# Kernel optimization log

Hardware: AMD Instinct MI355X
Metric: run time of the kernel (lower is better)

The kernel has to match this reference:

```python
import jax, jax.numpy as jnp
import numpy as np

EPS = 1e-12  # torch spectral_norm default eps


def _l2norm(v):
    return v / (jnp.linalg.norm(v) + EPS)


def _spectral_norm_2d(w, u):
    # one power iteration (torch default n_power_iterations=1), u/v detached
    v = _l2norm(w.T @ u)
    u_new = _l2norm(w @ v)
    u_new = jax.lax.stop_gradient(u_new)
    v = jax.lax.stop_gradient(v)
    sigma = u_new @ (w @ v)
    return w / sigma


def _spectral_norm_1d(b):
    # torch._SpectralNorm for ndim==1: F.normalize(weight, dim=0)
    return b / (jnp.linalg.norm(b) + EPS)


def setup_inputs() -> dict:
    key = jax.random.key(0)
    ks = jax.random.split(key, 8)
    T, B, I, H = 4096, 32, 256, 256
    s_i = 1.0 / np.sqrt(H)  # nn.RNN init: U(-1/sqrt(H), 1/sqrt(H))
    return {
        "x": jax.random.normal(ks[0], (T, B, I), jnp.float32),
        "state": jax.random.normal(ks[1], (1, B, H), jnp.float32),
        "w_ih": jax.random.uniform(ks[2], (H, I), jnp.float32, -s_i, s_i),
        "w_hh": jax.random.uniform(ks[3], (H, H), jnp.float32, -s_i, s_i),
        "b_ih": jax.random.uniform(ks[4], (H,), jnp.float32, -s_i, s_i),
        "b_hh": jax.random.uniform(ks[5], (H,), jnp.float32, -s_i, s_i),
        "u_ih": jax.random.normal(ks[6], (H,), jnp.float32),  # power-iteration buffer
        "u_hh": jax.random.normal(ks[7], (H,), jnp.float32),
    }


def reference(x, state, w_ih, w_hh, b_ih, b_hh, u_ih, u_hh):
    # spectral-norm parametrization of all RNN weights
    w_ih_sn = _spectral_norm_2d(w_ih, _l2norm(u_ih))
    w_hh_sn = _spectral_norm_2d(w_hh, _l2norm(u_hh))
    b_sn = _spectral_norm_1d(b_ih) + _spectral_norm_1d(b_hh)

    # input projection batched over all timesteps: [T,B,H]
    pre = jnp.einsum("tbi,hi->tbh", x, w_ih_sn) + b_sn

    def step(h, p):
        h_new = jnp.tanh(p + h @ w_hh_sn.T)
        return h_new, h_new

    h_last, out = jax.lax.scan(step, state[0], pre)
    return out, h_last[None]
```

## Files before the change

kernel.cpp:

```cpp
#include <hip/hip_runtime.h>
#include <hip/hip_bf16.h>
#include <math.h>

#define EPSF 1e-12f
#define H 256
#define TSTEPS 4096
#define BATCH 32
#define TB (TSTEPS*BATCH)
#define BH (BATCH*H)

typedef _Float16 h2 __attribute__((ext_vector_type(2)));

#if defined(__has_builtin)
#if __has_builtin(__builtin_amdgcn_fdot2)
#define FDOT2(a, b, c) __builtin_amdgcn_fdot2((a), (b), (c), false)
#endif
#endif
#ifndef FDOT2
#define FDOT2(a, b, c) fmaf((float)(a).y, (float)(b).y, fmaf((float)(a).x, (float)(b).x, (c)))
#endif

#define BC(u) __builtin_bit_cast(h2, (u))

#define DPPF(x, ctrl) __builtin_bit_cast(float, __builtin_amdgcn_update_dpp( \
    0, __builtin_bit_cast(int, (x)), (ctrl), 0xf, 0xf, true))
#define DPP_QUAD_XOR1 0xB1
#define DPP_QUAD_XOR2 0x4E
#define DPP_HALF_MIRROR 0x141
#define DPP_ROW_MIRROR  0x140

__device__ __forceinline__ void bar_nodrain() {
  __builtin_amdgcn_sched_barrier(0);
  asm volatile("s_waitcnt lgkmcnt(0)" ::: "memory");
  __builtin_amdgcn_s_barrier();
  __builtin_amdgcn_sched_barrier(0);
}

__device__ __forceinline__ float block_sum256(float v, float* red) {
  #pragma unroll
  for (int o = 32; o > 0; o >>= 1) v += __shfl_down(v, o, 64);
  __syncthreads();
  if ((threadIdx.x & 63) == 0) red[threadIdx.x >> 6] = v;
  __syncthreads();
  return red[0] + red[1] + red[2] + red[3];
}

__global__ __launch_bounds__(256) void k_prep(
    const float* __restrict__ w_ih, const float* __restrict__ w_hh,
    const float* __restrict__ b_ih, const float* __restrict__ b_hh,
    const float* __restrict__ u_ih, const float* __restrict__ u_hh,
    float* __restrict__ wsc) {
  __shared__ float red[4];
  __shared__ float ubuf[H];
  __shared__ float vbuf[H];
  const int tid = threadIdx.x;

  float inv_sig[2];
  const float* Ws[2] = {w_ih, w_hh};
  const float* Us[2] = {u_ih, u_hh};
  #pragma unroll 1
  for (int m = 0; m < 2; m++) {
    const float* W = Ws[m];
    float uv = Us[m][tid];
    float nu = sqrtf(block_sum256(uv * uv, red));
    ubuf[tid] = uv / (nu + EPSF);
    __syncthreads();
    float vt = 0.f;
    for (int h = 0; h < H; h++) vt = fmaf(W[h * H + tid], ubuf[h], vt);
    float nv = sqrtf(block_sum256(vt * vt, red));
    vbuf[tid] = vt / (nv + EPSF);
    __syncthreads();
    float wv = 0.f;
    const float* wr = W + (size_t)tid * H;
    for (int i = 0; i < H; i++) wv = fmaf(wr[i], vbuf[i], wv);
    float n2 = block_sum256(wv * wv, red);
    float sigma = n2 / (sqrtf(n2) + EPSF);
    inv_sig[m] = 1.f / sigma;
  }
  float bi = b_ih[tid], bh = b_hh[tid];
  float nbi = sqrtf(block_sum256(bi * bi, red));
  float nbh = sqrtf(block_sum256(bh * bh, red));
  wsc[tid] = bi / (nbi + EPSF) + bh / (nbh + EPSF);
  if (tid == 0) { wsc[H] = inv_sig[0]; wsc[H + 1] = inv_sig[1]; }
}

__global__ __launch_bounds__(256) void k_pre(
    const float* __restrict__ x, const float* __restrict__ w_ih,
    const float* __restrict__ wsc, float* __restrict__ pre) {
  __shared__ float xs[32 * 256];
  const int tid = threadIdx.x;
  const size_t m0 = (size_t)blockIdx.x * 32;

  const float4* xp = (const float4*)(x + m0 * H);
  float4* xsv = (float4*)xs;
  #pragma unroll
  for (int j = 0; j < 8; j++) xsv[j * 256 + tid] = xp[j * 256 + tid];
  __syncthreads();

  float acc[32];
  #pragma unroll
  for (int m = 0; m < 32; m++) acc[m] = 0.f;

  const float* wrow = w_ih + (size_t)tid * H;
  #pragma unroll 1
  for (int kb = 0; kb < 256; kb += 8) {
    float4 wa = *(const float4*)(wrow + kb);
    float4 wb = *(const float4*)(wrow + kb + 4);
    #pragma unroll
    for (int m = 0; m < 32; m++) {
      const float* xr = xs + m * 256 + kb;
      float4 xa = *(const float4*)xr;
      float4 xb = *(const float4*)(xr + 4);
      float a = acc[m];
      a = fmaf(xa.x, wa.x, a); a = fmaf(xa.y, wa.y, a);
      a = fmaf(xa.z, wa.z, a); a = fmaf(xa.w, wa.w, a);
      a = fmaf(xb.x, wb.x, a); a = fmaf(xb.y, wb.y, a);
      a = fmaf(xb.z, wb.z, a); a = fmaf(xb.w, wb.w, a);
      acc[m] = a;
    }
  }
  const float inv_s = wsc[H];
  const float bsn = wsc[tid];
  #pragma unroll
  for (int m = 0; m < 32; m++)
    pre[(m0 + m) * H + tid] = fmaf(acc[m], inv_s, bsn);
}

__device__ __forceinline__ int swz(int a) { return a ^ (((a >> 8) & 1) << 6); }

__global__ __launch_bounds__(512, 1) void k_scan(
    const float* __restrict__ state, const float* __restrict__ w_hh,
    const float* __restrict__ wsc, float* __restrict__ out) {
  __shared__ __align__(16) _Float16 hbuf[2][H];
  const int tid = threadIdx.x;
  const int cg   = tid >> 6;
  const int q    = tid & 63;
  const int rgrp = q >> 4;
  const int kseg = q & 15;
  const int jrow = 4 * ((q >> 3) & 1) + 2 * ((q >> 2) & 1) + ((q >> 1) & 1);
  const int myrow = (cg << 5) + (rgrp << 3) + jrow;
  const int b = blockIdx.x;
  const float inv_s = wsc[H + 1];
  const bool hb3 = (q >> 3) & 1, hb2 = (q >> 2) & 1, hb1 = (q >> 1) & 1;

  h2 wreg[8][8];
  #pragma unroll
  for (int i = 0; i < 8; i++) {
    const float* wr = w_hh + (size_t)((cg << 5) + (rgrp << 3) + i) * H + (kseg << 4);
    #pragma unroll
    for (int c = 0; c < 8; c++) {
      float2 wv = *(const float2*)(wr + 2 * c);
      wreg[i][c] = h2{(_Float16)(wv.x * inv_s), (_Float16)(wv.y * inv_s)};
    }
  }

  const int a0s = swz(kseg << 5);
  const int a1s = swz((kseg << 5) + 16);
  const int woff = swz(myrow * 2);

  if (tid < H)
    *(_Float16*)((char*)&hbuf[0][0] + swz(tid * 2)) = (_Float16)state[b * H + tid];

  const float* pbase = out + (size_t)b * H + myrow;
  float pre0 = pbase[0], pre1 = pbase[BH];
  bar_nodrain();

  float hn = 0.f;
  #pragma unroll 1
  for (int t = 0; t < TSTEPS; t++) {
    int tn = (t + 2 <= TSTEPS) ? (t + 2) : TSTEPS;
    float pre2 = pbase[(size_t)tn * BH];

    const char* hb = (const char*)&hbuf[t & 1][0];
    uint4 q0 = *(const uint4*)(hb + a0s);
    uint4 q1 = *(const uint4*)(hb + a1s);

    float acc[8];
    #pragma unroll
    for (int i = 0; i < 8; i++) {
      float a = 0.f;
      a = FDOT2(wreg[i][0], BC(q0.x), a);
      a = FDOT2(wreg[i][1], BC(q0.y), a);
      a = FDOT2(wreg[i][2], BC(q0.z), a);
      a = FDOT2(wreg[i][3], BC(q0.w), a);
      a = FDOT2(wreg[i][4], BC(q1.x), a);
      a = FDOT2(wreg[i][5], BC(q1.y), a);
      a = FDOT2(wreg[i][6], BC(q1.z), a);
      a = FDOT2(wreg[i][7], BC(q1.w), a);
      acc[i] = a;
    }

    float v0, v1, v2, v3;
    { float k0 = hb3 ? acc[4] : acc[0], s0 = hb3 ? acc[0] : acc[4];
      float k1 = hb3 ? acc[5] : acc[1], s1 = hb3 ? acc[1] : acc[5];
      float k2 = hb3 ? acc[6] : acc[2], s2 = hb3 ? acc[2] : acc[6];
      float k3 = hb3 ? acc[7] : acc[3], s3 = hb3 ? acc[3] : acc[7];
      v0 = k0 + DPPF(s0, DPP_ROW_MIRROR);
      v1 = k1 + DPPF(s1, DPP_ROW_MIRROR);
      v2 = k2 + DPPF(s2, DPP_ROW_MIRROR);
      v3 = k3 + DPPF(s3, DPP_ROW_MIRROR); }
    float u0, u1;
    { float k0 = hb2 ? v2 : v0, s0 = hb2 ? v0 : v2;
      float k1 = hb2 ? v3 : v1, s1 = hb2 ? v1 : v3;
      u0 = k0 + DPPF(s0, DPP_HALF_MIRROR);
      u1 = k1 + DPPF(s1, DPP_HALF_MIRROR); }
    float ssum;
    { float k0 = hb1 ? u1 : u0, s0 = hb1 ? u0 : u1;
      ssum = k0 + DPPF(s0, DPP_QUAD_XOR2); }
    ssum += DPPF(ssum, DPP_QUAD_XOR1);

    float s = ssum + pre0;
    float sc = fminf(fmaxf(s, -15.f), 15.f);
    float e = __expf(2.f * sc);
    hn = __fdividef(e - 1.f, e + 1.f);

    if (!(q & 1)) {
      *(_Float16*)((char*)&hbuf[(t + 1) & 1][0] + woff) = (_Float16)hn;
      out[(size_t)t * BH + b * H + myrow] = hn;
    }
    bar_nodrain();
    pre0 = pre1; pre1 = pre2;
  }
  if (!(q & 1)) out[(size_t)TSTEPS * BH + b * H + myrow] = hn;
}

extern "C" void kernel_launch(void* const* d_in, const int* in_sizes, int n_in,
                              void* d_out, int out_size, void* d_ws, size_t ws_size,
                              hipStream_t stream) {
  const float* x     = (const float*)d_in[0];
  const float* state = (const float*)d_in[1];
  const float* w_ih  = (const float*)d_in[2];
  const float* w_hh  = (const float*)d_in[3];
  const float* b_ih  = (const float*)d_in[4];
  const float* b_hh  = (const float*)d_in[5];
  const float* u_ih  = (const float*)d_in[6];
  const float* u_hh  = (const float*)d_in[7];
  float* out = (float*)d_out;
  float* wsc = (float*)d_ws;

  k_prep<<<1, 256, 0, stream>>>(w_ih, w_hh, b_ih, b_hh, u_ih, u_hh, wsc);
  k_pre<<<TB / 32, 256, 0, stream>>>(x, w_ih, wsc, out);
  k_scan<<<BATCH, 512, 0, stream>>>(state, w_hh, wsc, out);
}
```

Before: 2.728 ms.

## Use 8x8 register tiles with 64-row blocks in input projection GEMM

Restructures the k_pre input-projection GEMM so each thread computes an 8x8 output tile (8 rows by 8 hidden units) instead of one hidden unit across 32 rows, with 64 rows per block. This raises arithmetic intensity per LDS and global load and vectorizes the output stores. It doubles LDS usage to 64KB per block and raises register pressure, which may reduce occupancy. The sequential scan kernel, likely the dominant cost, is unchanged.

```diff
diff --git a/kernel.cpp b/kernel.cpp
--- a/kernel.cpp
+++ b/kernel.cpp
@@ -87,43 +87,67 @@
 __global__ __launch_bounds__(256) void k_pre(
     const float* __restrict__ x, const float* __restrict__ w_ih,
     const float* __restrict__ wsc, float* __restrict__ pre) {
-  __shared__ float xs[32 * 256];
+  __shared__ float xs[64 * 256];
   const int tid = threadIdx.x;
-  const size_t m0 = (size_t)blockIdx.x * 32;
+  const size_t m0 = (size_t)blockIdx.x * 64;
 
   const float4* xp = (const float4*)(x + m0 * H);
   float4* xsv = (float4*)xs;
   #pragma unroll
-  for (int j = 0; j < 8; j++) xsv[j * 256 + tid] = xp[j * 256 + tid];
+  for (int j = 0; j < 16; j++) xsv[j * 256 + tid] = xp[j * 256 + tid];
   __syncthreads();
 
-  float acc[32];
-  #pragma unroll
-  for (int m = 0; m < 32; m++) acc[m] = 0.f;
-
-  const float* wrow = w_ih + (size_t)tid * H;
+  const int hg = tid & 31;
+  const int mg = tid >> 5;
+  const int h0 = hg << 3;
+  const int mr0 = mg << 3;
+
+  float acc[8][8];
+  #pragma unroll
+  for (int i = 0; i < 8; i++)
+    #pragma unroll
+    for (int j = 0; j < 8; j++) acc[i][j] = 0.f;
+
+  const float* wbase = w_ih + (size_t)h0 * H;
   #pragma unroll 1
-  for (int kb = 0; kb < 256; kb += 8) {
-    float4 wa = *(const float4*)(wrow + kb);
-    float4 wb = *(const float4*)(wrow + kb + 4);
-    #pragma unroll
-    for (int m = 0; m < 32; m++) {
-      const float* xr = xs + m * 256 + kb;
-      float4 xa = *(const float4*)xr;
-      float4 xb = *(const float4*)(xr + 4);
-      float a = acc[m];
-      a = fmaf(xa.x, wa.x, a); a = fmaf(xa.y, wa.y, a);
-      a = fmaf(xa.z, wa.z, a); a = fmaf(xa.w, wa.w, a);
-      a = fmaf(xb.x, wb.x, a); a = fmaf(xb.y, wb.y, a);
-      a = fmaf(xb.z, wb.z, a); a = fmaf(xb.w, wb.w, a);
-      acc[m] = a;
+  for (int kb = 0; kb < 256; kb += 4) {
+    float4 w[8];
+    #pragma unroll
+    for (int j = 0; j < 8; j++)
+      w[j] = *(const float4*)(wbase + (size_t)j * H + kb);
+    #pragma unroll
+    for (int i = 0; i < 8; i++) {
+      float4 xv = *(const float4*)(xs + (mr0 + i) * 256 + kb);
+      #pragma unroll
+      for (int j = 0; j < 8; j++) {
+        float a = acc[i][j];
+        a = fmaf(xv.x, w[j].x, a);
+        a = fmaf(xv.y, w[j].y, a);
+        a = fmaf(xv.z, w[j].z, a);
+        a = fmaf(xv.w, w[j].w, a);
+        acc[i][j] = a;
+      }
     }
   }
   const float inv_s = wsc[H];
-  const float bsn = wsc[tid];
-  #pragma unroll
-  for (int m = 0; m < 32; m++)
-    pre[(m0 + m) * H + tid] = fmaf(acc[m], inv_s, bsn);
+  float bs[8];
+  #pragma unroll
+  for (int j = 0; j < 8; j++) bs[j] = wsc[h0 + j];
+  #pragma unroll
+  for (int i = 0; i < 8; i++) {
+    float4 o0, o1;
+    o0.x = fmaf(acc[i][0], inv_s, bs[0]);
+    o0.y = fmaf(acc[i][1], inv_s, bs[1]);
+    o0.z = fmaf(acc[i][2], inv_s, bs[2]);
+    o0.w = fmaf(acc[i][3], inv_s, bs[3]);
+    o1.x = fmaf(acc[i][4], inv_s, bs[4]);
+    o1.y = fmaf(acc[i][5], inv_s, bs[5]);
+    o1.z = fmaf(acc[i][6], inv_s, bs[6]);
+    o1.w = fmaf(acc[i][7], inv_s, bs[7]);
+    float* pr = pre + (m0 + mr0 + i) * H + h0;
+    *(float4*)pr = o0;
+    *(float4*)(pr + 4) = o1;
+  }
 }
 
 __device__ __forceinline__ int swz(int a) { return a ^ (((a >> 8) & 1) << 6); }
@@ -239,6 +263,6 @@
   float* wsc = (float*)d_ws;
 
   k_prep<<<1, 256, 0, stream>>>(w_ih, w_hh, b_ih, b_hh, u_ih, u_hh, wsc);
-  k_pre<<<TB / 32, 256, 0, stream>>>(x, w_ih, wsc, out);
+  k_pre<<<TB / 64, 256, 0, stream>>>(x, w_ih, wsc, out);
   k_scan<<<BATCH, 512, 0, stream>>>(state, w_hh, wsc, out);
 }
```

New measurement: 2.882 ms. +5.6%, slower.
